# Kernel optimization log

Hardware: AMD Instinct MI355X
Metric: run time of the kernel (lower is better)

## Reference

```python
import jax, jax.numpy as jnp
import numpy as np

T, B, H, I = 2048, 32, 1024, 1024

def setup_inputs() -> dict:
    key = jax.random.key(0)
    k1, k2, k3 = jax.random.split(key, 3)
    x = jax.random.normal(k1, (T, B, I), dtype=jnp.float32)
    # torch RNN default init: uniform(-1/sqrt(H), 1/sqrt(H))
    bound = 1.0 / np.sqrt(H)
    w_ih = jax.random.uniform(k2, (H, I), dtype=jnp.float32, minval=-bound, maxval=bound)
    b_ih = jnp.zeros((H,), dtype=jnp.float32)  # zeroed in IndRNN.__init__
    b_hh = jnp.zeros((H,), dtype=jnp.float32)
    # diagonal recurrent weight, uniform(-1, 1) per the module
    u = jax.random.uniform(k3, (H,), dtype=jnp.float32, minval=-1.0, maxval=1.0)
    return {"x": x, "w_ih": w_ih, "b_ih": b_ih, "b_hh": b_hh, "u": u}

def reference(x, w_ih, b_ih, b_hh, u):
    # Precompute input projection for all timesteps: [T, B, H]
    pre = jnp.einsum('tbi,hi->tbh', x, w_ih) + (b_ih + b_hh)

    def step(h, p):
        h_new = jax.nn.relu(p + u * h)  # diagonal recurrence: elementwise
        return h_new, h_new

    h0 = jnp.zeros((B, H), dtype=x.dtype)
    h_last, ys = jax.lax.scan(step, h0, pre)
    # Match torch.nn.RNN output: (output [T,B,H], h_n [1,B,H])
    return ys, h_last[None]
```

## Files before the change

### kernel.cpp

```cpp
#include <hip/hip_runtime.h>

#define T_DIM 2048
#define B_DIM 32
#define H_DIM 1024
#define I_DIM 1024
#define M_DIM (T_DIM * B_DIM)
#define K_DIM I_DIM
#define N_DIM H_DIM
#define YS_ELEMS (M_DIM * H_DIM)
#define BH (B_DIM * H_DIM)

typedef unsigned short u16;
typedef __attribute__((ext_vector_type(8))) short bf16x8;
typedef __attribute__((ext_vector_type(16))) float f32x16;

__device__ __forceinline__ u16 f2bf(float f) {
  union { float f; unsigned u; } c; c.f = f;
  return (u16)((c.u + 0x7fffu + ((c.u >> 16) & 1u)) >> 16);
}
__device__ __forceinline__ float bf2f(u16 s) {
  union { float f; unsigned u; } c; c.u = ((unsigned)s) << 16;
  return c.f;
}

__global__ __launch_bounds__(256) void split_kernel(
    const float* __restrict__ x, u16* __restrict__ hi, u16* __restrict__ lo, int n4) {
  int i = blockIdx.x * 256 + threadIdx.x;
  if (i >= n4) return;
  float4 v = ((const float4*)x)[i];
  ushort4 h, l;
  h.x = f2bf(v.x); l.x = f2bf(v.x - bf2f(h.x));
  h.y = f2bf(v.y); l.y = f2bf(v.y - bf2f(h.y));
  h.z = f2bf(v.z); l.z = f2bf(v.z - bf2f(h.z));
  h.w = f2bf(v.w); l.w = f2bf(v.w - bf2f(h.w));
  ((ushort4*)hi)[i] = h;
  ((ushort4*)lo)[i] = l;
}

__device__ __forceinline__ void gload_lds16(const u16* g, u16* l) {
  __builtin_amdgcn_global_load_lds(
      (const __attribute__((address_space(1))) void*)g,
      (__attribute__((address_space(3))) void*)l, 16, 0, 0);
}

#define WAITV0()    asm volatile("s_waitcnt vmcnt(0)" ::: "memory")
#define WAITLGKM0() asm volatile("s_waitcnt lgkmcnt(0)" ::: "memory")
#define BARX() do { asm volatile("" ::: "memory"); \
                    __builtin_amdgcn_s_barrier(); \
                    asm volatile("" ::: "memory"); } while (0)

__global__ __launch_bounds__(256, 3) void gemm_fused(
    const float* __restrict__ X, const u16* __restrict__ Wh,
    const u16* __restrict__ Wl, float* __restrict__ C) {
  __shared__ u16 sA[128 * 64];
  __shared__ u16 sB[2][128 * 64];

  const int tid = threadIdx.x;
  const int wave = tid >> 6;
  const int lane = tid & 63;
  const int cl = lane & 31;
  const int kh = lane >> 5;
  const int sx = lane & 7;

  const int bid = blockIdx.x;
  const int grp = bid >> 8;
  const int rr_ = bid & 255;
  const int n0 = (rr_ >> 5) * 128;
  const int m0 = ((grp << 5) + (rr_ & 31)) * 128;

  const u16* bsrc[4];
#pragma unroll
  for (int q = 0; q < 4; ++q) {
    const int rho = (q << 5) | (tid >> 3);
    const int slot = tid & 7;
    const int cc = slot ^ (rho & 7);
    const int pl = cc >> 2;
    const int c = cc & 3;
    bsrc[q] = (pl ? Wl : Wh) + (size_t)(n0 + rho) * K_DIM + (c << 3);
  }

  const int ar = tid >> 1;
  const int aseg = tid & 1;
  const float* xsrc = X + (size_t)(m0 + ar) * K_DIM + (aseg << 4);
  int awofs[2][2];
#pragma unroll
  for (int pl = 0; pl < 2; ++pl)
#pragma unroll
    for (int cq = 0; cq < 2; ++cq) {
      const int cc = (pl << 2) | (aseg << 1) | cq;
      awofs[pl][cq] = (ar << 6) + ((cc ^ (ar & 7)) << 3);
    }

  const int wm = (wave & 1) << 6;
  const int wn = (wave >> 1) << 6;
  int aRow[2], bRow[2];
#pragma unroll
  for (int i = 0; i < 2; ++i) {
    aRow[i] = (wm + (i << 5) + cl) << 6;
    bRow[i] = (wn + (i << 5) + cl) << 6;
  }
  int soH[2], soL[2];
#pragma unroll
  for (int s = 0; s < 2; ++s) {
    soH[s] = ((((s << 1) | kh)) ^ sx) << 3;
    soL[s] = (((4 | (s << 1) | kh)) ^ sx) << 3;
  }

  f32x16 acc[2][2] = {};

  float4 xv0 = ((const float4*)xsrc)[0];
  float4 xv1 = ((const float4*)xsrc)[1];
  float4 xv2 = ((const float4*)xsrc)[2];
  float4 xv3 = ((const float4*)xsrc)[3];
#pragma unroll
  for (int q = 0; q < 4; ++q)
    gload_lds16(bsrc[q], &sB[0][(q << 11) + (wave << 9)]);

#pragma unroll 1
  for (int k0 = 0; k0 < K_DIM; k0 += 32) {
    const int buf = (k0 >> 5) & 1;
    BARX();
    WAITV0();

    {
      float xf[16];
      *(float4*)(xf + 0) = xv0;  *(float4*)(xf + 4) = xv1;
      *(float4*)(xf + 8) = xv2;  *(float4*)(xf + 12) = xv3;
      u16 hh[16], ll[16];
#pragma unroll
      for (int e = 0; e < 16; ++e) {
        hh[e] = f2bf(xf[e]);
        ll[e] = f2bf(xf[e] - bf2f(hh[e]));
      }
#pragma unroll
      for (int cq = 0; cq < 2; ++cq) {
        bf16x8 hv, lv;
#pragma unroll
        for (int e = 0; e < 8; ++e) {
          hv[e] = (short)hh[cq * 8 + e];
          lv[e] = (short)ll[cq * 8 + e];
        }
        *(bf16x8*)(sA + awofs[0][cq]) = hv;
        *(bf16x8*)(sA + awofs[1][cq]) = lv;
      }
    }

    if (k0 + 32 < K_DIM) {
      const float* xs = xsrc + k0 + 32;
      xv0 = ((const float4*)xs)[0];
      xv1 = ((const float4*)xs)[1];
      xv2 = ((const float4*)xs)[2];
      xv3 = ((const float4*)xs)[3];
#pragma unroll
      for (int q = 0; q < 4; ++q)
        gload_lds16(bsrc[q] + k0 + 32, &sB[buf ^ 1][(q << 11) + (wave << 9)]);
    }

    WAITLGKM0();
    BARX();

    const u16* bb = &sB[buf][0];
#pragma unroll
    for (int s = 0; s < 2; ++s) {
      bf16x8 ah[2], al[2], bh[2], bl[2];
#pragma unroll
      for (int i = 0; i < 2; ++i) {
        ah[i] = *(const bf16x8*)(sA + aRow[i] + soH[s]);
        al[i] = *(const bf16x8*)(sA + aRow[i] + soL[s]);
        bh[i] = *(const bf16x8*)(bb + bRow[i] + soH[s]);
        bl[i] = *(const bf16x8*)(bb + bRow[i] + soL[s]);
      }
      __builtin_amdgcn_s_setprio(1);
#pragma unroll
      for (int i = 0; i < 2; ++i)
#pragma unroll
        for (int j = 0; j < 2; ++j) {
          acc[i][j] = __builtin_amdgcn_mfma_f32_32x32x16_bf16(ah[i], bh[j], acc[i][j], 0, 0, 0);
          acc[i][j] = __builtin_amdgcn_mfma_f32_32x32x16_bf16(ah[i], bl[j], acc[i][j], 0, 0, 0);
          acc[i][j] = __builtin_amdgcn_mfma_f32_32x32x16_bf16(al[i], bh[j], acc[i][j], 0, 0, 0);
        }
      __builtin_amdgcn_s_setprio(0);
    }
  }

  const int rh = (lane >> 5) * 4;
#pragma unroll
  for (int i = 0; i < 2; ++i)
#pragma unroll
    for (int j = 0; j < 2; ++j) {
      const int col = n0 + wn + j * 32 + cl;
      const size_t rb = (size_t)(m0 + wm + i * 32 + rh);
#pragma unroll
      for (int rr = 0; rr < 16; ++rr)
        C[(rb + (rr & 3) + 8 * (rr >> 2)) * N_DIM + col] = acc[i][j][rr];
    }
}

__global__ __launch_bounds__(64) void scan_kernel(
    float* __restrict__ yio, float* __restrict__ hlast,
    const float* __restrict__ bih, const float* __restrict__ bhh,
    const float* __restrict__ u) {
  const int j = blockIdx.x * 64 + threadIdx.x;
  const int hc = j & (H_DIM - 1);
  const float uu = u[hc];
  const float bias = bih[hc] + bhh[hc];
  float h = 0.f;
  float* p = yio + j;
  constexpr int UN = 64;
  float bufA[UN], bufB[UN];
#pragma unroll
  for (int i = 0; i < UN; ++i) bufA[i] = p[(size_t)i * BH];
#pragma unroll 1
  for (int t0 = 0; t0 < T_DIM; t0 += 2 * UN) {
#pragma unroll
    for (int i = 0; i < UN; ++i) bufB[i] = p[(size_t)(t0 + UN + i) * BH];
#pragma unroll
    for (int i = 0; i < UN; ++i) {
      float v = bufA[i] + bias + uu * h;
      h = v > 0.f ? v : 0.f;
      p[(size_t)(t0 + i) * BH] = h;
    }
    if (t0 + 2 * UN < T_DIM) {
#pragma unroll
      for (int i = 0; i < UN; ++i) bufA[i] = p[(size_t)(t0 + 2 * UN + i) * BH];
    }
#pragma unroll
    for (int i = 0; i < UN; ++i) {
      float v = bufB[i] + bias + uu * h;
      h = v > 0.f ? v : 0.f;
      p[(size_t)(t0 + UN + i) * BH] = h;
    }
  }
  hlast[j] = h;
}

extern "C" void kernel_launch(void* const* d_in, const int* in_sizes, int n_in,
                              void* d_out, int out_size, void* d_ws, size_t ws_size,
                              hipStream_t stream) {
  const float* x   = (const float*)d_in[0];
  const float* w   = (const float*)d_in[1];
  const float* bih = (const float*)d_in[2];
  const float* bhh = (const float*)d_in[3];
  const float* u   = (const float*)d_in[4];
  float* out = (float*)d_out;

  u16* wh = (u16*)d_ws;
  u16* wl = wh + (size_t)(H_DIM * I_DIM);

  split_kernel<<<(H_DIM * I_DIM) / 4 / 256, 256, 0, stream>>>(w, wh, wl, (H_DIM * I_DIM) / 4);
  gemm_fused<<<4096, 256, 0, stream>>>(x, wh, wl, out);
  scan_kernel<<<BH / 64, 64, 0, stream>>>(out, out + (size_t)YS_ELEMS, bih, bhh, u);
}
```

Baseline: 878.9 us.

## Software-pipeline GEMM main loop, rework LDS swizzle, use nontemporal memory ops

Restructures the fused GEMM loop so the fp32-to-bf16 hi/lo split of X for the next tile happens after the barrier, overlapped with MFMA compute on the current tile. It waits with vmcnt(4) instead of draining all loads, and adds a peeled epilogue iteration. The LDS XOR swizzle is changed to a permuted row/column mapping meant to cut bank conflicts for the new fragment ordering. Output stores in the GEMM and the scan's loads and stores become nontemporal to reduce cache pollution on the large streaming buffers. The partial vmcnt wait and swizzle changes carry correctness risk if counts or mappings are off.

```diff
diff --git a/kernel.cpp b/kernel.cpp
--- a/kernel.cpp
+++ b/kernel.cpp
@@ -43,6 +43,7 @@
       (__attribute__((address_space(3))) void*)l, 16, 0, 0);
 }
 
+#define WAITV4()    asm volatile("s_waitcnt vmcnt(4)" ::: "memory")
 #define WAITV0()    asm volatile("s_waitcnt vmcnt(0)" ::: "memory")
 #define WAITLGKM0() asm volatile("s_waitcnt lgkmcnt(0)" ::: "memory")
 #define BARX() do { asm volatile("" ::: "memory"); \
@@ -60,7 +61,6 @@
   const int lane = tid & 63;
   const int cl = lane & 31;
   const int kh = lane >> 5;
-  const int sx = lane & 7;
 
   const int bid = blockIdx.x;
   const int grp = bid >> 8;
@@ -73,22 +73,24 @@
   for (int q = 0; q < 4; ++q) {
     const int rho = (q << 5) | (tid >> 3);
     const int slot = tid & 7;
-    const int cc = slot ^ (rho & 7);
+    const int hr = (((rho & 3) << 1) | ((rho >> 2) & 1));
+    const int cc = slot ^ hr;
     const int pl = cc >> 2;
-    const int c = cc & 3;
-    bsrc[q] = (pl ? Wl : Wh) + (size_t)(n0 + rho) * K_DIM + (c << 3);
+    const int o = (((cc & 1) << 1) | ((cc >> 1) & 1));
+    bsrc[q] = (pl ? Wl : Wh) + (size_t)(n0 + rho) * K_DIM + (o << 3);
   }
 
   const int ar = tid >> 1;
   const int aseg = tid & 1;
   const float* xsrc = X + (size_t)(m0 + ar) * K_DIM + (aseg << 4);
+  const int har = (((ar & 3) << 1) | ((ar >> 2) & 1));
   int awofs[2][2];
 #pragma unroll
   for (int pl = 0; pl < 2; ++pl)
 #pragma unroll
     for (int cq = 0; cq < 2; ++cq) {
-      const int cc = (pl << 2) | (aseg << 1) | cq;
-      awofs[pl][cq] = (ar << 6) + ((cc ^ (ar & 7)) << 3);
+      const int cc = (pl << 2) | (cq << 1) | aseg;
+      awofs[pl][cq] = (ar << 6) + ((cc ^ har) << 3);
     }
 
   const int wm = (wave & 1) << 6;
@@ -99,89 +101,91 @@
     aRow[i] = (wm + (i << 5) + cl) << 6;
     bRow[i] = (wn + (i << 5) + cl) << 6;
   }
+  const int sx2 = (((cl & 3) << 1) | ((cl >> 2) & 1));
   int soH[2], soL[2];
 #pragma unroll
   for (int s = 0; s < 2; ++s) {
-    soH[s] = ((((s << 1) | kh)) ^ sx) << 3;
-    soL[s] = (((4 | (s << 1) | kh)) ^ sx) << 3;
+    soH[s] = ((((kh << 1) | s)) ^ sx2) << 3;
+    soL[s] = (((4 | (kh << 1) | s)) ^ sx2) << 3;
   }
 
   f32x16 acc[2][2] = {};
-
-  float4 xv0 = ((const float4*)xsrc)[0];
-  float4 xv1 = ((const float4*)xsrc)[1];
-  float4 xv2 = ((const float4*)xsrc)[2];
-  float4 xv3 = ((const float4*)xsrc)[3];
-#pragma unroll
-  for (int q = 0; q < 4; ++q)
-    gload_lds16(bsrc[q], &sB[0][(q << 11) + (wave << 9)]);
+  float4 xv0, xv1, xv2, xv3;
+  bf16x8 hv0, hv1, lv0, lv1;
+
+#define SPLIT_X() do { \
+    float xf[16]; \
+    *(float4*)(xf + 0) = xv0;  *(float4*)(xf + 4) = xv1; \
+    *(float4*)(xf + 8) = xv2;  *(float4*)(xf + 12) = xv3; \
+    u16 hh[16], ll[16]; \
+    _Pragma("unroll") for (int e = 0; e < 16; ++e) { \
+      hh[e] = f2bf(xf[e]); ll[e] = f2bf(xf[e] - bf2f(hh[e])); } \
+    _Pragma("unroll") for (int e = 0; e < 8; ++e) { \
+      hv0[e] = (short)hh[e];     lv0[e] = (short)ll[e]; \
+      hv1[e] = (short)hh[8 + e]; lv1[e] = (short)ll[8 + e]; } \
+  } while (0)
+
+#define LOAD_X(K0) do { const float* xs_ = xsrc + (K0); \
+    xv0 = ((const float4*)xs_)[0]; xv1 = ((const float4*)xs_)[1]; \
+    xv2 = ((const float4*)xs_)[2]; xv3 = ((const float4*)xs_)[3]; } while (0)
+
+#define WRITE_A() do { \
+    *(bf16x8*)(sA + awofs[0][0]) = hv0; *(bf16x8*)(sA + awofs[0][1]) = hv1; \
+    *(bf16x8*)(sA + awofs[1][0]) = lv0; *(bf16x8*)(sA + awofs[1][1]) = lv1; \
+  } while (0)
+
+#define STAGE_B(K0, NB) do { \
+    _Pragma("unroll") for (int q = 0; q < 4; ++q) \
+      gload_lds16(bsrc[q] + (K0), &sB[NB][(q << 11) + (wave << 9)]); \
+  } while (0)
+
+#define COMPUTE(BUF) do { \
+    const u16* bb_ = &sB[BUF][0]; \
+    _Pragma("unroll") for (int s = 0; s < 2; ++s) { \
+      bf16x8 ah[2], al[2], bh[2], bl[2]; \
+      _Pragma("unroll") for (int i = 0; i < 2; ++i) { \
+        ah[i] = *(const bf16x8*)(sA + aRow[i] + soH[s]); \
+        al[i] = *(const bf16x8*)(sA + aRow[i] + soL[s]); \
+        bh[i] = *(const bf16x8*)(bb_ + bRow[i] + soH[s]); \
+        bl[i] = *(const bf16x8*)(bb_ + bRow[i] + soL[s]); \
+      } \
+      __builtin_amdgcn_s_setprio(1); \
+      _Pragma("unroll") for (int i = 0; i < 2; ++i) \
+      _Pragma("unroll") for (int j = 0; j < 2; ++j) { \
+        acc[i][j] = __builtin_amdgcn_mfma_f32_32x32x16_bf16(ah[i], bh[j], acc[i][j], 0, 0, 0); \
+        acc[i][j] = __builtin_amdgcn_mfma_f32_32x32x16_bf16(ah[i], bl[j], acc[i][j], 0, 0, 0); \
+        acc[i][j] = __builtin_amdgcn_mfma_f32_32x32x16_bf16(al[i], bh[j], acc[i][j], 0, 0, 0); \
+      } \
+      __builtin_amdgcn_s_setprio(0); \
+    } \
+  } while (0)
+
+  STAGE_B(0, 0);
+  LOAD_X(0);
+  SPLIT_X();
+  LOAD_X(32);
 
 #pragma unroll 1
-  for (int k0 = 0; k0 < K_DIM; k0 += 32) {
+  for (int k0 = 0; k0 < K_DIM - 32; k0 += 32) {
     const int buf = (k0 >> 5) & 1;
     BARX();
-    WAITV0();
-
-    {
-      float xf[16];
-      *(float4*)(xf + 0) = xv0;  *(float4*)(xf + 4) = xv1;
-      *(float4*)(xf + 8) = xv2;  *(float4*)(xf + 12) = xv3;
-      u16 hh[16], ll[16];
-#pragma unroll
-      for (int e = 0; e < 16; ++e) {
-        hh[e] = f2bf(xf[e]);
-        ll[e] = f2bf(xf[e] - bf2f(hh[e]));
-      }
-#pragma unroll
-      for (int cq = 0; cq < 2; ++cq) {
-        bf16x8 hv, lv;
-#pragma unroll
-        for (int e = 0; e < 8; ++e) {
-          hv[e] = (short)hh[cq * 8 + e];
-          lv[e] = (short)ll[cq * 8 + e];
-        }
-        *(bf16x8*)(sA + awofs[0][cq]) = hv;
-        *(bf16x8*)(sA + awofs[1][cq]) = lv;
-      }
-    }
-
-    if (k0 + 32 < K_DIM) {
-      const float* xs = xsrc + k0 + 32;
-      xv0 = ((const float4*)xs)[0];
-      xv1 = ((const float4*)xs)[1];
-      xv2 = ((const float4*)xs)[2];
-      xv3 = ((const float4*)xs)[3];
-#pragma unroll
-      for (int q = 0; q < 4; ++q)
-        gload_lds16(bsrc[q] + k0 + 32, &sB[buf ^ 1][(q << 11) + (wave << 9)]);
-    }
-
+    WAITV4();
+    WRITE_A();
     WAITLGKM0();
     BARX();
-
-    const u16* bb = &sB[buf][0];
-#pragma unroll
-    for (int s = 0; s < 2; ++s) {
-      bf16x8 ah[2], al[2], bh[2], bl[2];
-#pragma unroll
-      for (int i = 0; i < 2; ++i) {
-        ah[i] = *(const bf16x8*)(sA + aRow[i] + soH[s]);
-        al[i] = *(const bf16x8*)(sA + aRow[i] + soL[s]);
-        bh[i] = *(const bf16x8*)(bb + bRow[i] + soH[s]);
-        bl[i] = *(const bf16x8*)(bb + bRow[i] + soL[s]);
-      }
-      __builtin_amdgcn_s_setprio(1);
-#pragma unroll
-      for (int i = 0; i < 2; ++i)
-#pragma unroll
-        for (int j = 0; j < 2; ++j) {
-          acc[i][j] = __builtin_amdgcn_mfma_f32_32x32x16_bf16(ah[i], bh[j], acc[i][j], 0, 0, 0);
-          acc[i][j] = __builtin_amdgcn_mfma_f32_32x32x16_bf16(ah[i], bl[j], acc[i][j], 0, 0, 0);
-          acc[i][j] = __builtin_amdgcn_mfma_f32_32x32x16_bf16(al[i], bh[j], acc[i][j], 0, 0, 0);
-        }
-      __builtin_amdgcn_s_setprio(0);
-    }
-  }
+    STAGE_B(k0 + 32, buf ^ 1);
+    __builtin_amdgcn_sched_barrier(0);
+    SPLIT_X();
+    if (k0 + 64 < K_DIM) LOAD_X(k0 + 64);
+    COMPUTE(buf);
+  }
+
+  BARX();
+  WAITV0();
+  WRITE_A();
+  WAITLGKM0();
+  BARX();
+  COMPUTE(1);
 
   const int rh = (lane >> 5) * 4;
 #pragma unroll
@@ -192,8 +196,14 @@
       const size_t rb = (size_t)(m0 + wm + i * 32 + rh);
 #pragma unroll
       for (int rr = 0; rr < 16; ++rr)
-        C[(rb + (rr & 3) + 8 * (rr >> 2)) * N_DIM + col] = acc[i][j][rr];
-    }
+        __builtin_nontemporal_store(acc[i][j][rr],
+            &C[(rb + (rr & 3) + 8 * (rr >> 2)) * N_DIM + col]);
+    }
+#undef SPLIT_X
+#undef LOAD_X
+#undef WRITE_A
+#undef STAGE_B
+#undef COMPUTE
 }
 
 __global__ __launch_bounds__(64) void scan_kernel(
@@ -209,26 +219,28 @@
   constexpr int UN = 64;
   float bufA[UN], bufB[UN];
 #pragma unroll
-  for (int i = 0; i < UN; ++i) bufA[i] = p[(size_t)i * BH];
+  for (int i = 0; i < UN; ++i) bufA[i] = __builtin_nontemporal_load(&p[(size_t)i * BH]);
 #pragma unroll 1
   for (int t0 = 0; t0 < T_DIM; t0 += 2 * UN) {
 #pragma unroll
-    for (int i = 0; i < UN; ++i) bufB[i] = p[(size_t)(t0 + UN + i) * BH];
+    for (int i = 0; i < UN; ++i)
+      bufB[i] = __builtin_nontemporal_load(&p[(size_t)(t0 + UN + i) * BH]);
 #pragma unroll
     for (int i = 0; i < UN; ++i) {
       float v = bufA[i] + bias + uu * h;
       h = v > 0.f ? v : 0.f;
-      p[(size_t)(t0 + i) * BH] = h;
+      __builtin_nontemporal_store(h, &p[(size_t)(t0 + i) * BH]);
     }
     if (t0 + 2 * UN < T_DIM) {
 #pragma unroll
-      for (int i = 0; i < UN; ++i) bufA[i] = p[(size_t)(t0 + 2 * UN + i) * BH];
+      for (int i = 0; i < UN; ++i)
+        bufA[i] = __builtin_nontemporal_load(&p[(size_t)(t0 + 2 * UN + i) * BH]);
     }
 #pragma unroll
     for (int i = 0; i < UN; ++i) {
       float v = bufB[i] + bias + uu * h;
       h = v > 0.f ? v : 0.f;
-      p[(size_t)(t0 + UN + i) * BH] = h;
+      __builtin_nontemporal_store(h, &p[(size_t)(t0 + UN + i) * BH]);
     }
   }
   hlast[j] = h;
```

Measured after the change: 877.9 us. Within noise of the previous version (-0.1%).
